# Kernel tuning notes

Hardware: AMD Instinct MI355X
Metric: run time of the kernel (lower is better)

The kernel has to match this reference:

```python
import jax, jax.numpy as jnp
import numpy as np
from functools import partial

CONF_THRESH = 0.01
NMS_THRESH = 0.45
TOP_K = 200


def setup_inputs() -> dict:
    key = jax.random.key(0)
    k1, k2, k3 = jax.random.split(key, 3)
    B, N, C = 256, 8732, 21
    loc_data = jax.random.normal(k1, (B, N, 4), dtype=jnp.float32)
    conf_data = jax.random.normal(k2, (B, N, C), dtype=jnp.float32)
    dbox_list = jax.random.uniform(k3, (N, 4), dtype=jnp.float32)
    return {"loc_data": loc_data, "conf_data": conf_data, "dbox_list": dbox_list}


def decode(loc, dbox):
    # loc, dbox: (N, 4). Faithful to torch decode: variances 0.1 / 0.2.
    cxcy = dbox[:, :2] + loc[:, :2] * 0.1 * dbox[:, 2:]
    wh = dbox[:, 2:] * jnp.exp(loc[:, 2:] * 0.2)
    xymin = cxcy - wh / 2.0
    xymax = xymin + wh
    return jnp.concatenate([xymin, xymax], axis=1)  # (N,4) xmin,ymin,xmax,ymax


def nms_single(boxes, scores):
    # boxes: (N,4), scores: (N,). Returns (TOP_K, 5) rows [conf, x1, y1, x2, y2]
    # compacted to the front in descending-score keep order (matches torch output[i,cl,:count]).
    masked = jnp.where(scores > CONF_THRESH, scores, -1.0)
    top_scores, top_idx = jax.lax.top_k(masked, TOP_K)
    b = boxes[top_idx]  # (TOP_K, 4)
    x1, y1, x2, y2 = b[:, 0], b[:, 1], b[:, 2], b[:, 3]
    area = (x2 - x1) * (y2 - y1)
    valid = top_scores > CONF_THRESH

    def body(i, state):
        suppressed, keep = state
        active = jnp.logical_not(suppressed[i])
        keep = keep.at[i].set(active)
        # Faithful to source: all four coords are clamped with min=coord[i]
        # (i.e. elementwise max), including x2/y2 -- reproducing the original math.
        xx1 = jnp.maximum(x1, x1[i])
        yy1 = jnp.maximum(y1, y1[i])
        xx2 = jnp.maximum(x2, x2[i])
        yy2 = jnp.maximum(y2, y2[i])
        inter = (xx2 - xx1) * (yy2 - yy1)
        union = area - inter + area[i]
        iou = inter / union
        sup_new = jnp.logical_and(active, iou > NMS_THRESH)
        sup_new = sup_new.at[i].set(False)
        return jnp.logical_or(suppressed, sup_new), keep

    suppressed0 = jnp.logical_not(valid)
    keep0 = jnp.zeros((TOP_K,), dtype=bool)
    suppressed, keep = jax.lax.fori_loop(0, TOP_K, body, (suppressed0, keep0))

    rows = jnp.concatenate([top_scores[:, None], b], axis=1)  # (TOP_K, 5)
    rows = jnp.where(keep[:, None], rows, 0.0)
    dest = jnp.where(keep, jnp.cumsum(keep) - 1, TOP_K)  # dump slot TOP_K
    out = jnp.zeros((TOP_K + 1, 5), dtype=boxes.dtype).at[dest].set(rows)
    return out[:TOP_K]


def reference(loc_data, conf_data, dbox_list):
    # loc_data: (B, 8732, 4); conf_data: (B, 8732, 21); dbox_list: (8732, 4)
    conf = jax.nn.softmax(conf_data, axis=-1)          # (B, N, C)
    conf_preds = jnp.transpose(conf, (0, 2, 1))        # (B, C, N)
    decoded = jax.vmap(decode, in_axes=(0, None))(loc_data, dbox_list)  # (B, N, 4)
    per_class = jax.vmap(lambda bx, sc: jax.vmap(lambda s: nms_single(bx, s))(sc))(
        decoded, conf_preds
    )  # (B, C, TOP_K, 5)
    # class 0 is background and is skipped in the torch loop -> zeros
    return per_class.at[:, 0].set(0.0)
```

## Files before the change

### kernel.cpp

```cpp
#include <hip/hip_runtime.h>
#include <cstdint>

#pragma clang fp contract(off)

#define TPB 256
typedef unsigned int uint32;
typedef unsigned short u16;
typedef unsigned long long u64;

constexpr int BB = 256;
constexpr int NN = 8732;
constexpr int CC = 21;
constexpr int KK = 200;
constexpr int CH = (NN + TPB - 1) / TPB;
constexpr uint32 KBIAS = 0x3C23D70Au;

__device__ __forceinline__ double fexp(double a) {
  const double L2E = 1.4426950408889634074;
  const double SHIFT = 6755399441055744.0;
  double t = __builtin_fma(a, L2E, SHIFT);
  int i = (int)__double_as_longlong(t);
  double n = t - SHIFT;
  double r = __builtin_fma(n, -6.93147180369123816490e-01, a);
  r = __builtin_fma(n, -1.90821492927058770002e-10, r);
  double p = 1.6059043836821614599e-10;
  p = __builtin_fma(p, r, 2.0876756987868098979e-9);
  p = __builtin_fma(p, r, 2.5052108385441718775e-8);
  p = __builtin_fma(p, r, 2.7557319223985890653e-7);
  p = __builtin_fma(p, r, 2.7557319223985890653e-6);
  p = __builtin_fma(p, r, 2.4801587301587301587e-5);
  p = __builtin_fma(p, r, 1.9841269841269841270e-4);
  p = __builtin_fma(p, r, 1.3888888888888888889e-3);
  p = __builtin_fma(p, r, 8.3333333333333333333e-3);
  p = __builtin_fma(p, r, 4.1666666666666666667e-2);
  p = __builtin_fma(p, r, 1.6666666666666666667e-1);
  p = __builtin_fma(p, r, 0.5);
  p = __builtin_fma(p, r, 1.0);
  p = __builtin_fma(p, r, 1.0);
  return p * __longlong_as_double((long long)(1023 + i) << 52);
}

struct NmsS {
  alignas(16) float bx1[256];
  alignas(16) float by1[256];
  alignas(16) float bx2[256];
  alignas(16) float by2[256];
  alignas(16) float barea[256];
  alignas(16) float bscore[256];
  alignas(16) u64 mask[KK][4];
  u64 kept[4];
};
struct SmemT {
  union alignas(16) UU {
    u16 s16[NN];
    NmsS nms;
  } u;
  uint32 hist[512];
  alignas(16) u64 cand[256];
  uint32 sc4[4];
  uint32 bc[3];
  uint32 slot;
};
static_assert(sizeof(SmemT) <= 22 * 1024, "LDS budget for 7 blocks/CU");

__device__ __forceinline__ uint32 kk_of(float p) {
  return (p > 0.01f) ? (__float_as_uint(p) - KBIAS) : 0u;
}

__device__ __forceinline__ void scan_find(SmemT& sm, uint32 target, int t, int lane, int wv,
                                          uint32& pivot, uint32& cntabove, uint32& pivcnt,
                                          uint32& total) {
  uint32 h0 = sm.hist[2 * t], h1 = sm.hist[2 * t + 1];
  uint32 part = h0 + h1;
  uint32 suf = part;
  for (int off = 1; off < 64; off <<= 1) {
    uint32 v = __shfl_down(suf, off, 64);
    if (lane + off < 64) suf += v;
  }
  if (lane == 0) sm.sc4[wv] = suf;
  __syncthreads();
  uint32 tot = sm.sc4[0] + sm.sc4[1] + sm.sc4[2] + sm.sc4[3];
  uint32 add = 0;
  for (int w = wv + 1; w < 4; ++w) add += sm.sc4[w];
  uint32 mine = suf + add, nxt = mine - part;
  if (mine >= target && nxt < target) {
    uint32 acc = nxt + h1;
    if (acc >= target) { sm.bc[0] = 2u * t + 1u; sm.bc[1] = nxt; sm.bc[2] = h1; }
    else               { sm.bc[0] = 2u * t;      sm.bc[1] = acc; sm.bc[2] = h0; }
  }
  __syncthreads();
  sm.hist[2 * t] = 0u;
  sm.hist[2 * t + 1] = 0u;
  pivot = sm.bc[0];
  cntabove = sm.bc[1];
  pivcnt = sm.bc[2];
  total = tot;
  __syncthreads();
}

template <int MODE>
__global__ __launch_bounds__(TPB, 5) void prep_kernel(const float* __restrict__ conf,
                                                      float* __restrict__ probsT,
                                                      double2* __restrict__ ms) {
  __shared__ float tile[TPB * CC];
  const int blk = blockIdx.x;
  const int b = blockIdx.y;
  const int n0 = blk * TPB;
  const int cnt = (NN - n0 < TPB) ? (NN - n0) : TPB;
  const size_t base = ((size_t)b * NN + n0) * CC;
  if (cnt == TPB) {
    const float4* s4 = (const float4*)(conf + base);
    float4* t4 = (float4*)tile;
    for (int i = threadIdx.x; i < (TPB * CC) / 4; i += TPB) t4[i] = s4[i];
  } else {
    for (int i = threadIdx.x; i < cnt * CC; i += TPB) tile[i] = conf[base + i];
  }
  __syncthreads();
  if (threadIdx.x >= cnt) return;
  const int n = n0 + threadIdx.x;
  const float* cp = tile + threadIdx.x * CC;
  float mx = cp[0];
#pragma unroll
  for (int j = 1; j < CC; ++j) mx = fmaxf(mx, cp[j]);
  const double mxd = (double)mx;

  if (MODE == 0) {
    double es1[CC - 1];
    double S = fexp((double)cp[0] - mxd);
#pragma unroll
    for (int j = 1; j < CC; ++j) {
      es1[j - 1] = fexp((double)cp[j] - mxd);
      S += es1[j - 1];
    }
    const double Sinv = 1.0 / S;
    const double EBH = 1.0 + 3e-14, EBL = 1.0 - 3e-14;
    bool slow = false;
    float* op = probsT + (size_t)b * 20 * NN + n;
#pragma unroll
    for (int c2 = 1; c2 < CC; ++c2) {
      double ph = es1[c2 - 1] * Sinv;
      if ((float)(ph * EBH) != (float)(ph * EBL)) slow = true;
      op[(size_t)(c2 - 1) * NN] = (float)ph;
    }
    if (__builtin_expect(slow, 0)) {
      double es2[CC];
      double S2 = 0.0;
      for (int j = 0; j < CC; ++j) {
        es2[j] = exp((double)cp[j] - mxd);
        S2 += es2[j];
      }
      double Si2 = 1.0 / S2;
      for (int c2 = 1; c2 < CC; ++c2) op[(size_t)(c2 - 1) * NN] = (float)(es2[c2] * Si2);
    }
  } else {
    double S = 0.0;
#pragma unroll
    for (int j = 0; j < CC; ++j) S += exp((double)cp[j] - mxd);
    ms[(size_t)b * NN + n] = make_double2(mxd, 1.0 / S);
  }
}

template <int MODE>
__device__ __forceinline__ float prob_one(const float* __restrict__ prow,
                                          const float* __restrict__ conf,
                                          const double2* __restrict__ ms,
                                          int b, int c, int n) {
  if (MODE == 0) {
    return prow[n];
  } else if (MODE == 1) {
    double2 mv = ms[(size_t)b * NN + n];
    float x = conf[((size_t)b * NN + n) * CC + c];
    return (float)(exp((double)x - mv.x) * mv.y);
  } else {
    const float* cp = conf + ((size_t)b * NN + n) * CC;
    float mx = cp[0];
    for (int j = 1; j < CC; ++j) mx = fmaxf(mx, cp[j]);
    double S = 0.0, ec = 0.0;
    for (int j = 0; j < CC; ++j) {
      double e = exp((double)cp[j] - (double)mx);
      S += e;
      if (j == c) ec = e;
    }
    return (float)(ec * (1.0 / S));
  }
}

template <int MODE>
__global__ __launch_bounds__(TPB, 7) void nms_kernel(
    const float* __restrict__ probsT, const float* __restrict__ conf,
    const double2* __restrict__ ms, const float* __restrict__ loc,
    const float* __restrict__ dbox, float* __restrict__ out) {
  __shared__ SmemT sm;
  const int t = threadIdx.x;
  const int lane = t & 63;
  const int wv = t >> 6;
  const int tb = blockIdx.x;
  const int xcd = tb & 7;
  const int s0i = tb >> 3;
  const int bi = s0i / CC;
  const int c = s0i - bi * CC;
  const int b = bi * 8 + xcd;
  const size_t outbase = (size_t)(b * CC + c) * KK * 5;

  if (c == 0) {
    for (int i = t; i < KK * 5; i += TPB) out[outbase + i] = 0.0f;
    return;
  }
  const float* prow = (MODE == 0) ? probsT + ((size_t)b * 20 + (c - 1)) * NN : nullptr;

  sm.hist[t] = 0u;
  sm.hist[t + 256] = 0u;
  if (t == 0) sm.slot = 0u;
  __syncthreads();

  if (MODE == 0) {
    const float4* p4 = (const float4*)prow;
    for (int i = t; i < NN / 4; i += TPB) {
      float4 p = p4[i];
      uint32 k0 = kk_of(p.x), k1 = kk_of(p.y), k2 = kk_of(p.z), k3 = kk_of(p.w);
      uint32 s0 = k0 ? (k0 >> 10) + 1u : 0u;
      uint32 s1 = k1 ? (k1 >> 10) + 1u : 0u;
      uint32 s2 = k2 ? (k2 >> 10) + 1u : 0u;
      uint32 s3 = k3 ? (k3 >> 10) + 1u : 0u;
      ((u64*)sm.u.s16)[i] = (u64)s0 | ((u64)s1 << 16) | ((u64)s2 << 32) | ((u64)s3 << 48);
      if (s0) atomicAdd(&sm.hist[s0 >> 8], 1u);
      if (s1) atomicAdd(&sm.hist[s1 >> 8], 1u);
      if (s2) atomicAdd(&sm.hist[s2 >> 8], 1u);
      if (s3) atomicAdd(&sm.hist[s3 >> 8], 1u);
    }
  } else {
    for (int n = t; n < NN; n += TPB) {
      uint32 k = kk_of(prob_one<MODE>(prow, conf, ms, b, c, n));
      uint32 s = k ? (k >> 10) + 1u : 0u;
      sm.u.s16[n] = (u16)s;
      if (s) atomicAdd(&sm.hist[s >> 8], 1u);
    }
  }
  __syncthreads();
  uint32 P0, cg0, pc0, total;
  scan_find(sm, (uint32)KK, t, lane, wv, P0, cg0, pc0, total);

  const bool few = total < (uint32)KK;
  uint32 P16, cgA = 0, eqc = 0, ncand;
  if (!few) {
    for (int i = t; i < NN / 2; i += TPB) {
      uint32 w = ((const uint32*)sm.u.s16)[i];
      uint32 a = w & 0xFFFFu, bq = w >> 16;
      if ((a >> 8) == P0) atomicAdd(&sm.hist[a & 0xFFu], 1u);
      if ((bq >> 8) == P0) atomicAdd(&sm.hist[bq & 0xFFu], 1u);
    }
    __syncthreads();
    uint32 P1, cg1, pc1, tot1;
    scan_find(sm, (uint32)KK - cg0, t, lane, wv, P1, cg1, pc1, tot1);
    P16 = (P0 << 8) | P1;
    cgA = cg0 + cg1;
    eqc = pc1;
    ncand = cgA + eqc;
  } else {
    P16 = 1u;
    ncand = total;
  }

  u64 val = 0;
  if (ncand <= 256u) {
    sm.cand[t] = 0ull;
    __syncthreads();
    for (int i = t; i < NN / 2; i += TPB) {
      uint32 w = ((const uint32*)sm.u.s16)[i];
      uint32 a = w & 0xFFFFu, bq = w >> 16;
      if (a >= P16) { uint32 s = atomicAdd(&sm.slot, 1u); sm.cand[s] = (u64)(2 * i); }
      if (bq >= P16) { uint32 s = atomicAdd(&sm.slot, 1u); sm.cand[s] = (u64)(2 * i + 1); }
    }
    __syncthreads();
    if (few) {
      const int base = t * CH;
      const int endn = (base + CH < NN) ? (base + CH) : NN;
      uint32 cz = 0;
      for (int n = base; n < endn; ++n) cz += (sm.u.s16[n] == 0);
      uint32 incl = cz;
      for (int off = 1; off < 64; off <<= 1) {
        uint32 v = __shfl_up(incl, off, 64);
        if (lane >= off) incl += v;
      }
      if (lane == 63) sm.sc4[wv] = incl;
      __syncthreads();
      uint32 add = 0;
      for (int w2 = 0; w2 < wv; ++w2) add += sm.sc4[w2];
      uint32 g = add + incl - cz;
      const uint32 npad = (uint32)KK - ncand;
      if (cz && g < npad) {
        for (int n = base; n < endn && g < npad; ++n)
          if (sm.u.s16[n] == 0) { sm.cand[ncand + g] = (u64)n; ++g; }
      }
      __syncthreads();
    }
    const uint32 ntot = few ? (uint32)KK : ncand;
    if (t < (int)ntot) {
      uint32 idx = (uint32)sm.cand[t];
      uint32 k = (t < (int)ncand) ? kk_of(prob_one<MODE>(prow, conf, ms, b, c, (int)idx)) : 0u;
      val = ((u64)k << 32) | (uint32)(~idx);
    }
  } else {
    const uint32 BK = P16 - 1u;
    const uint32 tgt = (uint32)KK - cgA;
    for (int n = t; n < NN; n += TPB) {
      uint32 k = kk_of(prob_one<MODE>(prow, conf, ms, b, c, n));
      if (k && (k >> 10) == BK) atomicAdd(&sm.hist[(k >> 5) & 31u], 1u);
    }
    __syncthreads();
    uint32 q0, d0, px, tx;
    scan_find(sm, tgt, t, lane, wv, q0, d0, px, tx);
    for (int n = t; n < NN; n += TPB) {
      uint32 k = kk_of(prob_one<MODE>(prow, conf, ms, b, c, n));
      if (k && (k >> 5) == ((BK << 5) | q0)) atomicAdd(&sm.hist[k & 31u], 1u);
    }
    __syncthreads();
    uint32 q1, d1, py, ty;
    scan_find(sm, tgt - d0, t, lane, wv, q1, d1, py, ty);
    const uint32 T = (BK << 10) | (q0 << 5) | q1;
    const uint32 cnt_gt = cgA + d0 + d1;
    const uint32 m_need = (uint32)KK - cnt_gt;
    sm.cand[t] = 0ull;
    if (t == 0) sm.slot = 0u;
    __syncthreads();
    const int base = t * CH;
    const int endn = (base + CH < NN) ? (base + CH) : NN;
    uint32 cnteq = 0;
    for (int n = base; n < endn; ++n) {
      uint32 k = kk_of(prob_one<MODE>(prow, conf, ms, b, c, n));
      if (k > T) {
        uint32 s = atomicAdd(&sm.slot, 1u);
        sm.cand[s] = ((u64)k << 32) | (uint32)(~(uint32)n);
      }
      cnteq += (k == T);
    }
    uint32 incl = cnteq;
    for (int off = 1; off < 64; off <<= 1) {
      uint32 v = __shfl_up(incl, off, 64);
      if (lane >= off) incl += v;
    }
    if (lane == 63) sm.sc4[wv] = incl;
    __syncthreads();
    uint32 add = 0;
    for (int w2 = 0; w2 < wv; ++w2) add += sm.sc4[w2];
    uint32 g = add + incl - cnteq;
    if (cnteq && g < m_need) {
      for (int n = base; n < endn && g < m_need; ++n) {
        uint32 k = kk_of(prob_one<MODE>(prow, conf, ms, b, c, n));
        if (k == T) {
          sm.cand[cnt_gt + g] = ((u64)T << 32) | (uint32)(~(uint32)n);
          ++g;
        }
      }
    }
    __syncthreads();
    val = sm.cand[t];
  }

  for (int kk = 2; kk <= 256; kk <<= 1) {
    for (int j = kk >> 1; j > 0; j >>= 1) {
      u64 other;
      if (j >= 64) {
        __syncthreads();
        sm.cand[t] = val;
        __syncthreads();
        other = sm.cand[t ^ j];
      } else {
        other = __shfl_xor((unsigned long long)val, j, 64);
      }
      const bool takeMax = ((t & kk) == 0) == ((t & j) == 0);
      val = takeMax ? (val > other ? val : other) : (val < other ? val : other);
    }
  }
  __syncthreads();

  if (t < KK) {
    uint32 k32 = (uint32)(val >> 32);
    uint32 idx = ~((uint32)val);
    bool valid = k32 != 0u;
    float score = valid ? __uint_as_float(k32 + KBIAS) : -1.0f;
    const float4 lc = ((const float4*)loc)[(size_t)b * NN + idx];
    const float4 db = ((const float4*)dbox)[idx];
    float cx = db.x + (lc.x * 0.1f) * db.z;
    float cy = db.y + (lc.y * 0.1f) * db.w;
    float w_ = db.z * (float)exp((double)(lc.z * 0.2f));
    float h_ = db.w * (float)exp((double)(lc.w * 0.2f));
    float x1 = cx - w_ * 0.5f;
    float y1 = cy - h_ * 0.5f;
    float x2 = x1 + w_;
    float y2 = y1 + h_;
    sm.u.nms.bx1[t] = x1;
    sm.u.nms.by1[t] = y1;
    sm.u.nms.bx2[t] = x2;
    sm.u.nms.by2[t] = y2;
    sm.u.nms.barea[t] = (x2 - x1) * (y2 - y1);
    sm.u.nms.bscore[t] = score;
  } else {
    sm.u.nms.bscore[t] = -1.0f;
  }
  __syncthreads();

  if (t < KK) {
    const double MD = 0x1.CCCCCDp-2;
    const float xi1 = sm.u.nms.bx1[t], yi1 = sm.u.nms.by1[t];
    const float xi2 = sm.u.nms.bx2[t], yi2 = sm.u.nms.by2[t];
    const float ai = sm.u.nms.barea[t];
    const int wq0 = t >> 6;
#pragma unroll
    for (int wq = 0; wq < 4; ++wq) {
      if (wq < wq0) { sm.u.nms.mask[t][wq] = 0; continue; }
      const int jbeg = wq * 64;
      const int jend = (jbeg + 64 < KK) ? (jbeg + 64) : KK;
      u64 w = 0;
      for (int j0 = jbeg; j0 < jend; j0 += 4) {
        const float4 q1 = *(const float4*)&sm.u.nms.bx1[j0];
        const float4 q2 = *(const float4*)&sm.u.nms.by1[j0];
        const float4 q3 = *(const float4*)&sm.u.nms.bx2[j0];
        const float4 q4 = *(const float4*)&sm.u.nms.by2[j0];
        const float4 qa = *(const float4*)&sm.u.nms.barea[j0];
        const float a1[4] = {q1.x, q1.y, q1.z, q1.w};
        const float a2[4] = {q2.x, q2.y, q2.z, q2.w};
        const float a3[4] = {q3.x, q3.y, q3.z, q3.w};
        const float a4[4] = {q4.x, q4.y, q4.z, q4.w};
        const float aa[4] = {qa.x, qa.y, qa.z, qa.w};
#pragma unroll
        for (int e = 0; e < 4; ++e) {
          const int j = j0 + e;
          float xx1 = fmaxf(a1[e], xi1);
          float yy1 = fmaxf(a2[e], yi1);
          float xx2 = fmaxf(a3[e], xi2);
          float yy2 = fmaxf(a4[e], yi2);
          float inter = (xx2 - xx1) * (yy2 - yy1);
          float uni = (aa[e] - inter) + ai;
          bool sup = (uni > 0.0f) ? ((double)inter > MD * (double)uni)
                                  : (uni == 0.0f && inter > 0.0f);
          if (sup && j > t) w |= 1ull << (j & 63);
        }
      }
      sm.u.nms.mask[t][wq] = w;
    }
  }
  __syncthreads();

  if (wv == 0) {
    u64 s0 = __ballot(!(sm.u.nms.bscore[lane] > 0.01f));
    u64 s1 = __ballot(!(sm.u.nms.bscore[64 + lane] > 0.01f));
    u64 s2 = __ballot(!(sm.u.nms.bscore[128 + lane] > 0.01f));
    u64 s3 = __ballot(!(sm.u.nms.bscore[192 + lane] > 0.01f)) | ~0xFFull;
    u64 k0 = 0, k1 = 0, k2 = 0, k3 = 0;
    const u64(*M)[4] = sm.u.nms.mask;
    u64 n0 = M[0][0], n1 = M[0][1], n2 = M[0][2], n3 = M[0][3];
    int i = 0;
#define WALK_BLOCK(SW, KW, CNT)                                          \
  for (int ii = 0; ii < (CNT); ++ii, ++i) {                              \
    u64 c0 = n0, c1 = n1, c2 = n2, c3 = n3;                              \
    if (i + 1 < KK) {                                                    \
      n0 = M[i + 1][0]; n1 = M[i + 1][1];                                \
      n2 = M[i + 1][2]; n3 = M[i + 1][3];                                \
    }                                                                    \
    u64 bm = 1ull << ii;                                                 \
    if (!((SW) & bm)) {                                                  \
      (KW) |= bm;                                                        \
      s0 |= c0; s1 |= c1; s2 |= c2; s3 |= c3;                            \
    }                                                                    \
  }
    WALK_BLOCK(s0, k0, 64)
    WALK_BLOCK(s1, k1, 64)
    WALK_BLOCK(s2, k2, 64)
    WALK_BLOCK(s3, k3, 8)
#undef WALK_BLOCK
    if (lane == 0) {
      sm.u.nms.kept[0] = k0; sm.u.nms.kept[1] = k1;
      sm.u.nms.kept[2] = k2; sm.u.nms.kept[3] = k3;
    }
  }
  __syncthreads();

  if (t < KK) {
    const u64 K0 = sm.u.nms.kept[0], K1 = sm.u.nms.kept[1];
    const u64 K2 = sm.u.nms.kept[2], K3 = sm.u.nms.kept[3];
    const int w = t >> 6;
    const int bit = t & 63;
    u64 kw = (w == 0) ? K0 : (w == 1) ? K1 : (w == 2) ? K2 : K3;
    bool kp = (kw >> bit) & 1ull;
    int nk = __popcll(K0) + __popcll(K1) + __popcll(K2) + __popcll(K3);
    if (kp) {
      u64 lowm = (bit == 0) ? 0ull : (~0ull >> (64 - bit));
      int d = __popcll(kw & lowm);
      if (w > 0) d += __popcll(K0);
      if (w > 1) d += __popcll(K1);
      if (w > 2) d += __popcll(K2);
      float* o = out + outbase + (size_t)d * 5;
      o[0] = sm.u.nms.bscore[t];
      o[1] = sm.u.nms.bx1[t];
      o[2] = sm.u.nms.by1[t];
      o[3] = sm.u.nms.bx2[t];
      o[4] = sm.u.nms.by2[t];
    }
    if (t >= nk) {
      float* o = out + outbase + (size_t)t * 5;
      o[0] = 0.f; o[1] = 0.f; o[2] = 0.f; o[3] = 0.f; o[4] = 0.f;
    }
  }
}

extern "C" void kernel_launch(void* const* d_in, const int* in_sizes, int n_in,
                              void* d_out, int out_size, void* d_ws, size_t ws_size,
                              hipStream_t stream) {
  (void)in_sizes; (void)n_in; (void)out_size;
  const float* loc = (const float*)d_in[0];
  const float* conf = (const float*)d_in[1];
  const float* dbox = (const float*)d_in[2];
  float* out = (float*)d_out;

  const size_t needA = (size_t)BB * 20 * NN * sizeof(float);
  const size_t needB = (size_t)BB * NN * sizeof(double2);
  dim3 blk(TPB);
  dim3 g1((NN + TPB - 1) / TPB, BB);
  const int g2 = BB * CC;

  if (ws_size >= needA) {
    float* probsT = (float*)d_ws;
    prep_kernel<0><<<g1, blk, 0, stream>>>(conf, probsT, nullptr);
    nms_kernel<0><<<g2, blk, 0, stream>>>(probsT, conf, nullptr, loc, dbox, out);
  } else if (ws_size >= needB) {
    double2* msp = (double2*)d_ws;
    prep_kernel<1><<<g1, blk, 0, stream>>>(conf, nullptr, msp);
    nms_kernel<1><<<g2, blk, 0, stream>>>(nullptr, conf, msp, loc, dbox, out);
  } else {
    nms_kernel<2><<<g2, blk, 0, stream>>>(nullptr, conf, nullptr, loc, dbox, out);
  }
}
```

Before: 505.3 us.

## Rebalance NMS mask work across threads and deepen walk prefetch

Spreads the upper-triangular IoU mask computation over all 256 threads in 64-wide units so that threads 200-255 also do work and per-thread load is more even. The serial keep walk now prefetches mask rows eight deep through a register ring instead of one row ahead. While wave 0 walks, the other waves zero-fill the output with float4 stores, and the softmax ambiguity check uses cheaper integer bit tests, with prep occupancy raised to 6. The risks are more register pressure in the walk, prefetch reads past row 199 into whatever follows the mask in shared memory, and a write-after-write ordering between the zero fill and the kept-row stores that depends on the barrier.

```diff
diff --git a/kernel.cpp b/kernel.cpp
--- a/kernel.cpp
+++ b/kernel.cpp
@@ -99,7 +99,7 @@
 }
 
 template <int MODE>
-__global__ __launch_bounds__(TPB, 5) void prep_kernel(const float* __restrict__ conf,
+__global__ __launch_bounds__(TPB, 6) void prep_kernel(const float* __restrict__ conf,
                                                       float* __restrict__ probsT,
                                                       double2* __restrict__ ms) {
   __shared__ float tile[TPB * CC];
@@ -133,13 +133,14 @@
       S += es1[j - 1];
     }
     const double Sinv = 1.0 / S;
-    const double EBH = 1.0 + 3e-14, EBL = 1.0 - 3e-14;
     bool slow = false;
     float* op = probsT + (size_t)b * 20 * NN + n;
 #pragma unroll
     for (int c2 = 1; c2 < CC; ++c2) {
       double ph = es1[c2 - 1] * Sinv;
-      if ((float)(ph * EBH) != (float)(ph * EBL)) slow = true;
+      uint32 low29 = (uint32)__double_as_longlong(ph) & 0x1FFFFFFFu;
+      uint32 dist = (low29 > 0x10000000u) ? (low29 - 0x10000000u) : (0x10000000u - low29);
+      slow = slow || (dist <= 320u) || (ph < 1e-30);
       op[(size_t)(c2 - 1) * NN] = (float)ph;
     }
     if (__builtin_expect(slow, 0)) {
@@ -183,6 +184,42 @@
     }
     return (float)(ec * (1.0 / S));
   }
+}
+
+__device__ __forceinline__ void mask_unit(NmsS& nm, int r, int wq, int jcnt) {
+  const double MD = 0x1.CCCCCDp-2;
+  const float xi1 = nm.bx1[r], yi1 = nm.by1[r];
+  const float xi2 = nm.bx2[r], yi2 = nm.by2[r];
+  const float ai = nm.barea[r];
+  const int jbeg = wq * 64;
+  u64 w = 0;
+#pragma unroll 4
+  for (int j0 = jbeg; j0 < jbeg + jcnt; j0 += 4) {
+    const float4 q1 = *(const float4*)&nm.bx1[j0];
+    const float4 q2 = *(const float4*)&nm.by1[j0];
+    const float4 q3 = *(const float4*)&nm.bx2[j0];
+    const float4 q4 = *(const float4*)&nm.by2[j0];
+    const float4 qa = *(const float4*)&nm.barea[j0];
+    const float a1[4] = {q1.x, q1.y, q1.z, q1.w};
+    const float a2[4] = {q2.x, q2.y, q2.z, q2.w};
+    const float a3[4] = {q3.x, q3.y, q3.z, q3.w};
+    const float a4[4] = {q4.x, q4.y, q4.z, q4.w};
+    const float aa[4] = {qa.x, qa.y, qa.z, qa.w};
+#pragma unroll
+    for (int e = 0; e < 4; ++e) {
+      const int j = j0 + e;
+      float xx1 = fmaxf(a1[e], xi1);
+      float yy1 = fmaxf(a2[e], yi1);
+      float xx2 = fmaxf(a3[e], xi2);
+      float yy2 = fmaxf(a4[e], yi2);
+      float inter = (xx2 - xx1) * (yy2 - yy1);
+      float uni = (aa[e] - inter) + ai;
+      bool sup = (uni > 0.0f) ? ((double)inter > MD * (double)uni)
+                              : (uni == 0.0f && inter > 0.0f);
+      if (sup && j > r) w |= 1ull << (j & 63);
+    }
+  }
+  nm.mask[r][wq] = w;
 }
 
 template <int MODE>
@@ -400,45 +437,16 @@
   }
   __syncthreads();
 
-  if (t < KK) {
-    const double MD = 0x1.CCCCCDp-2;
-    const float xi1 = sm.u.nms.bx1[t], yi1 = sm.u.nms.by1[t];
-    const float xi2 = sm.u.nms.bx2[t], yi2 = sm.u.nms.by2[t];
-    const float ai = sm.u.nms.barea[t];
-    const int wq0 = t >> 6;
-#pragma unroll
-    for (int wq = 0; wq < 4; ++wq) {
-      if (wq < wq0) { sm.u.nms.mask[t][wq] = 0; continue; }
-      const int jbeg = wq * 64;
-      const int jend = (jbeg + 64 < KK) ? (jbeg + 64) : KK;
-      u64 w = 0;
-      for (int j0 = jbeg; j0 < jend; j0 += 4) {
-        const float4 q1 = *(const float4*)&sm.u.nms.bx1[j0];
-        const float4 q2 = *(const float4*)&sm.u.nms.by1[j0];
-        const float4 q3 = *(const float4*)&sm.u.nms.bx2[j0];
-        const float4 q4 = *(const float4*)&sm.u.nms.by2[j0];
-        const float4 qa = *(const float4*)&sm.u.nms.barea[j0];
-        const float a1[4] = {q1.x, q1.y, q1.z, q1.w};
-        const float a2[4] = {q2.x, q2.y, q2.z, q2.w};
-        const float a3[4] = {q3.x, q3.y, q3.z, q3.w};
-        const float a4[4] = {q4.x, q4.y, q4.z, q4.w};
-        const float aa[4] = {qa.x, qa.y, qa.z, qa.w};
-#pragma unroll
-        for (int e = 0; e < 4; ++e) {
-          const int j = j0 + e;
-          float xx1 = fmaxf(a1[e], xi1);
-          float yy1 = fmaxf(a2[e], yi1);
-          float xx2 = fmaxf(a3[e], xi2);
-          float yy2 = fmaxf(a4[e], yi2);
-          float inter = (xx2 - xx1) * (yy2 - yy1);
-          float uni = (aa[e] - inter) + ai;
-          bool sup = (uni > 0.0f) ? ((double)inter > MD * (double)uni)
-                                  : (uni == 0.0f && inter > 0.0f);
-          if (sup && j > t) w |= 1ull << (j & 63);
-        }
-      }
-      sm.u.nms.mask[t][wq] = w;
-    }
+  {
+    int u1 = t;
+    int wqa = (u1 < 64) ? 0 : (u1 < 192) ? 1 : 2;
+    int ra = (u1 < 64) ? u1 : (u1 < 192) ? (u1 - 64) : (u1 - 192);
+    mask_unit(sm.u.nms, ra, wqa, 64);
+    if (t >= 128) {
+      int rb = (t - 128) + 64;
+      mask_unit(sm.u.nms, rb, 2, 64);
+    }
+    if (t < KK) mask_unit(sm.u.nms, t, 3, 8);
   }
   __syncthreads();
 
@@ -449,30 +457,39 @@
     u64 s3 = __ballot(!(sm.u.nms.bscore[192 + lane] > 0.01f)) | ~0xFFull;
     u64 k0 = 0, k1 = 0, k2 = 0, k3 = 0;
     const u64(*M)[4] = sm.u.nms.mask;
-    u64 n0 = M[0][0], n1 = M[0][1], n2 = M[0][2], n3 = M[0][3];
-    int i = 0;
-#define WALK_BLOCK(SW, KW, CNT)                                          \
-  for (int ii = 0; ii < (CNT); ++ii, ++i) {                              \
-    u64 c0 = n0, c1 = n1, c2 = n2, c3 = n3;                              \
-    if (i + 1 < KK) {                                                    \
-      n0 = M[i + 1][0]; n1 = M[i + 1][1];                                \
-      n2 = M[i + 1][2]; n3 = M[i + 1][3];                                \
-    }                                                                    \
+    u64 pre[8][4];
+#pragma unroll
+    for (int s = 0; s < 8; ++s) {
+      pre[s][0] = M[s][0]; pre[s][1] = M[s][1];
+      pre[s][2] = M[s][2]; pre[s][3] = M[s][3];
+    }
+#define WALK_BLOCK(SW, KW, CNT, IBASE)                                   \
+  _Pragma("unroll 8")                                                    \
+  for (int ii = 0; ii < (CNT); ++ii) {                                   \
+    const int s = ii & 7;                                                \
+    u64 c0 = pre[s][0], c1 = pre[s][1], c2 = pre[s][2], c3 = pre[s][3];  \
+    const int inext = (IBASE) + ii + 8;                                  \
+    pre[s][0] = M[inext][0]; pre[s][1] = M[inext][1];                    \
+    pre[s][2] = M[inext][2]; pre[s][3] = M[inext][3];                    \
     u64 bm = 1ull << ii;                                                 \
     if (!((SW) & bm)) {                                                  \
       (KW) |= bm;                                                        \
       s0 |= c0; s1 |= c1; s2 |= c2; s3 |= c3;                            \
     }                                                                    \
   }
-    WALK_BLOCK(s0, k0, 64)
-    WALK_BLOCK(s1, k1, 64)
-    WALK_BLOCK(s2, k2, 64)
-    WALK_BLOCK(s3, k3, 8)
+    WALK_BLOCK(s0, k0, 64, 0)
+    WALK_BLOCK(s1, k1, 64, 64)
+    WALK_BLOCK(s2, k2, 64, 128)
+    WALK_BLOCK(s3, k3, 8, 192)
 #undef WALK_BLOCK
     if (lane == 0) {
       sm.u.nms.kept[0] = k0; sm.u.nms.kept[1] = k1;
       sm.u.nms.kept[2] = k2; sm.u.nms.kept[3] = k3;
     }
+  } else {
+    float4 z4 = make_float4(0.f, 0.f, 0.f, 0.f);
+    float4* o4 = (float4*)(out + outbase);
+    for (int i = t - 64; i < (KK * 5) / 4; i += 192) o4[i] = z4;
   }
   __syncthreads();
 
@@ -483,7 +500,6 @@
     const int bit = t & 63;
     u64 kw = (w == 0) ? K0 : (w == 1) ? K1 : (w == 2) ? K2 : K3;
     bool kp = (kw >> bit) & 1ull;
-    int nk = __popcll(K0) + __popcll(K1) + __popcll(K2) + __popcll(K3);
     if (kp) {
       u64 lowm = (bit == 0) ? 0ull : (~0ull >> (64 - bit));
       int d = __popcll(kw & lowm);
@@ -497,10 +513,6 @@
       o[3] = sm.u.nms.bx2[t];
       o[4] = sm.u.nms.by2[t];
     }
-    if (t >= nk) {
-      float* o = out + outbase + (size_t)t * 5;
-      o[0] = 0.f; o[1] = 0.f; o[2] = 0.f; o[3] = 0.f; o[4] = 0.f;
-    }
   }
 }
 
```

Result: faster. 493.4 us (-2.3%).
